# Kernel optimization log

Hardware: AMD Instinct MI355X
Metric: run time of the kernel (lower is better)

Reference implementation:

```python
import jax, jax.numpy as jnp
import numpy as np

N = 50000      # nodes
E = 800000     # edges (before self-loops)
IN_DIM = 128
HID = 96
PROJ = 64
BN_EPS = 1e-5
L2_EPS = 1e-12


def setup_inputs() -> dict:
    key = jax.random.key(0)
    ks = jax.random.split(key, 8)

    def glorot(k, shape):
        fan_in, fan_out = shape
        s = np.sqrt(6.0 / (fan_in + fan_out)).astype(np.float32)
        return jax.random.uniform(k, shape, jnp.float32, -s, s)

    x = jax.random.normal(ks[0], (N, IN_DIM), jnp.float32)
    edge_index = jax.random.randint(ks[1], (2, E), 0, N, dtype=jnp.int64)

    return {
        "x": x,
        "edge_index": edge_index,
        # GCN layer 1
        "W1": glorot(ks[2], (IN_DIM, HID)), "b1": jnp.zeros(HID, jnp.float32),
        "g1": jnp.ones(HID, jnp.float32), "be1": jnp.zeros(HID, jnp.float32),
        # GCN layer 2
        "W2": glorot(ks[3], (HID, HID)), "b2": jnp.zeros(HID, jnp.float32),
        "g2": jnp.ones(HID, jnp.float32), "be2": jnp.zeros(HID, jnp.float32),
        # projector: Linear -> BN -> ReLU -> Linear
        "Wp1": glorot(ks[4], (HID, HID)), "bp1": jnp.zeros(HID, jnp.float32),
        "gp": jnp.ones(HID, jnp.float32), "bep": jnp.zeros(HID, jnp.float32),
        "Wp2": glorot(ks[5], (HID, PROJ)), "bp2": jnp.zeros(PROJ, jnp.float32),
    }


def _batchnorm(h, gamma, beta):
    # training-mode BatchNorm1d: batch stats, biased variance
    m = h.mean(axis=0)
    v = h.var(axis=0)
    return gamma * (h - m) * jax.lax.rsqrt(v + BN_EPS) + beta


def _gcn_conv(x, W, b, src, dst, deg_inv_sqrt):
    # PyG GCNConv: x @ W, symmetric-normalized scatter-add (self-loops included
    # in src/dst), then bias.
    xw = x @ W                                              # [N, out]
    norm = deg_inv_sqrt[src] * deg_inv_sqrt[dst]            # [E+N]
    msg = xw[src] * norm[:, None]                           # [E+N, out]
    out = jax.ops.segment_sum(msg, dst, num_segments=x.shape[0])
    return out + b


def reference(x, edge_index, W1, b1, g1, be1, W2, b2, g2, be2,
              Wp1, bp1, gp, bep, Wp2, bp2):
    n = x.shape[0]
    loops = jnp.arange(n, dtype=edge_index.dtype)
    src = jnp.concatenate([edge_index[0], loops])
    dst = jnp.concatenate([edge_index[1], loops])
    deg = jax.ops.segment_sum(jnp.ones(src.shape[0], x.dtype), dst,
                              num_segments=n)               # includes self-loops
    deg_inv_sqrt = jax.lax.rsqrt(deg)                       # deg >= 1 always

    h = jax.nn.relu(_batchnorm(_gcn_conv(x, W1, b1, src, dst, deg_inv_sqrt), g1, be1))
    h = jax.nn.relu(_batchnorm(_gcn_conv(h, W2, b2, src, dst, deg_inv_sqrt), g2, be2))

    z = jax.nn.relu(_batchnorm(h @ Wp1 + bp1, gp, bep))
    z = z @ Wp2 + bp2
    # F.normalize(p=2, dim=-1, eps=1e-12)
    nrm = jnp.linalg.norm(z, axis=-1, keepdims=True)
    return z / jnp.maximum(nrm, L2_EPS)
```

## Files before the change

### kernel.cpp

```cpp
#include <hip/hip_runtime.h>
#include <hip/hip_fp16.h>

constexpr int BLK = 256;

static inline int cdiv(long long a, int b) { return (int)((a + b - 1) / b); }

using v8h = __attribute__((ext_vector_type(8))) _Float16;
using v4f = __attribute__((ext_vector_type(4))) float;


__global__ void zero_int(int* __restrict__ p, int n) {
    for (int i = blockIdx.x * blockDim.x + threadIdx.x; i < n; i += gridDim.x * blockDim.x)
        p[i] = 0;
}


__global__ void count_dst_off(const int* __restrict__ dst, int* __restrict__ cnt,
                              unsigned short* __restrict__ eoff, int E) {
    for (int i = blockIdx.x * blockDim.x + threadIdx.x; i < E; i += gridDim.x * blockDim.x)
        eoff[i] = (unsigned short)atomicAdd(&cnt[dst[i]], 1);
}

__global__ void scan1_dis(const int* __restrict__ cnt, int* __restrict__ rowptr,
                          int* __restrict__ bsum, float* __restrict__ dis, int N) {
    __shared__ int ts[256];
    int tid = threadIdx.x;
    int base = blockIdx.x * 1024 + tid * 4;
    int v[4], s = 0;
#pragma unroll
    for (int i = 0; i < 4; ++i) {
        v[i] = (base + i < N) ? cnt[base + i] : 0;
        s += v[i];
        if (base + i < N) dis[base + i] = rsqrtf((float)v[i] + 1.0f);
    }
    ts[tid] = s;
    __syncthreads();
    for (int off = 1; off < 256; off <<= 1) {
        int t = 0;
        if (tid >= off) t = ts[tid - off];
        __syncthreads();
        if (tid >= off) ts[tid] += t;
        __syncthreads();
    }
    int run = ts[tid] - s;
#pragma unroll
    for (int i = 0; i < 4; ++i) {
        if (base + i < N) rowptr[base + i] = run;
        run += v[i];
    }
    if (tid == 255) bsum[blockIdx.x] = ts[255];
}

__global__ void scan2z(const int* __restrict__ bsum, int* __restrict__ boff, int nb,
                       float* __restrict__ sums) {
    int tid = threadIdx.x;
    if (tid < 64) {
        int orig = (tid < nb) ? bsum[tid] : 0;
        int v = orig;
#pragma unroll
        for (int off = 1; off < 64; off <<= 1) {
            int t = __shfl_up(v, off, 64);
            if (tid >= off) v += t;
        }
        if (tid < nb) boff[tid] = v - orig;
    } else if (tid < 64 + 576) {
        sums[tid - 64] = 0.0f;
    }
}

__global__ void scan3(int* __restrict__ rowptr, const int* __restrict__ boff, int N, int E) {
    int i = blockIdx.x * blockDim.x + threadIdx.x;
    if (i < N) rowptr[i] += boff[i >> 10];
    if (i == 0) rowptr[N] = E;
}

__global__ void csr_fill(const int* __restrict__ src, const int* __restrict__ dst,
                         const unsigned short* __restrict__ eoff,
                         const int* __restrict__ rowptr,
                         unsigned short* __restrict__ csrc, int E) {
    for (int i = blockIdx.x * blockDim.x + threadIdx.x; i < E; i += gridDim.x * blockDim.x) {
        csrc[rowptr[dst[i]] + (int)eoff[i]] = (unsigned short)src[i];
    }
}


template <int K, bool ACT, bool BIAS, bool HOUT, bool WOUT, bool STATS>
__global__ __launch_bounds__(256) void gemm96m(const float* __restrict__ in,
                                               const float* __restrict__ W,
                                               const float* __restrict__ bias,
                                               const float* __restrict__ bnsums,
                                               const float* __restrict__ gamma,
                                               const float* __restrict__ beta,
                                               const float* __restrict__ dsc,
                                               float* __restrict__ out,
                                               _Float16* __restrict__ hout,
                                               float* __restrict__ osums, int N) {
    constexpr int NK = K / 32;
    constexpr int LDK = K + 8;
    __shared__ __align__(16) _Float16 Wt[96 * LDK];
    __shared__ __align__(16) float ssl[ACT ? 192 : 1];
    __shared__ float sb[STATS ? 192 : 1];
    const int tid = threadIdx.x;
    for (int idx = tid; idx < K * 96; idx += 256) {
        int k = idx / 96, n = idx - k * 96;
        Wt[n * LDK + k] = (_Float16)W[idx];
    }
    if (ACT && tid < 96) {
        float inv_n = 1.0f / (float)N;
        float mean = bnsums[tid] * inv_n;
        float var = bnsums[96 + tid] * inv_n - mean * mean;
        float sc = gamma[tid] * rsqrtf(var + 1e-5f);
        ssl[tid] = sc;
        ssl[96 + tid] = beta[tid] - mean * sc;
    }
    if (STATS && tid < 192) sb[tid] = 0.0f;
    __syncthreads();

    const int wave = tid >> 6, lane = tid & 63;
    const int quad = lane >> 4, lm = lane & 15;
    const int rbase = blockIdx.x * 64 + wave * 16;
    int arow = rbase + lm;
    arow = arow < N ? arow : N - 1;

    v8h afr[NK];
#pragma unroll
    for (int kc = 0; kc < NK; ++kc) {
        const float* p = &in[(long long)arow * K + kc * 32 + quad * 8];
        float4 p0 = *(const float4*)p;
        float4 p1 = *(const float4*)(p + 4);
        if (ACT) {
            int kk = kc * 32 + quad * 8;
            float4 sc0 = *(const float4*)&ssl[kk];
            float4 sc1 = *(const float4*)&ssl[kk + 4];
            float4 sh0 = *(const float4*)&ssl[96 + kk];
            float4 sh1 = *(const float4*)&ssl[96 + kk + 4];
            p0.x = fmaxf(fmaf(p0.x, sc0.x, sh0.x), 0.0f);
            p0.y = fmaxf(fmaf(p0.y, sc0.y, sh0.y), 0.0f);
            p0.z = fmaxf(fmaf(p0.z, sc0.z, sh0.z), 0.0f);
            p0.w = fmaxf(fmaf(p0.w, sc0.w, sh0.w), 0.0f);
            p1.x = fmaxf(fmaf(p1.x, sc1.x, sh1.x), 0.0f);
            p1.y = fmaxf(fmaf(p1.y, sc1.y, sh1.y), 0.0f);
            p1.z = fmaxf(fmaf(p1.z, sc1.z, sh1.z), 0.0f);
            p1.w = fmaxf(fmaf(p1.w, sc1.w, sh1.w), 0.0f);
        }
        v8h a;
        a[0] = (_Float16)p0.x; a[1] = (_Float16)p0.y;
        a[2] = (_Float16)p0.z; a[3] = (_Float16)p0.w;
        a[4] = (_Float16)p1.x; a[5] = (_Float16)p1.y;
        a[6] = (_Float16)p1.z; a[7] = (_Float16)p1.w;
        afr[kc] = a;
    }

    v4f acc[6];
#pragma unroll
    for (int t = 0; t < 6; ++t) {
        v4f c = {0.0f, 0.0f, 0.0f, 0.0f};
#pragma unroll
        for (int kc = 0; kc < NK; ++kc) {
            v8h b = *(const v8h*)&Wt[(t * 16 + lm) * LDK + kc * 32 + quad * 8];
            c = __builtin_amdgcn_mfma_f32_16x16x32_f16(afr[kc], b, c, 0, 0, 0);
        }
        acc[t] = c;
    }

    float dr[4];
    if (HOUT) {
#pragma unroll
        for (int r = 0; r < 4; ++r) {
            int gr = rbase + quad * 4 + r;
            dr[r] = dsc[gr < N ? gr : N - 1];
        }
    }

    float ls[6], lq[6];
#pragma unroll
    for (int t = 0; t < 6; ++t) { ls[t] = 0.0f; lq[t] = 0.0f; }
#pragma unroll
    for (int t = 0; t < 6; ++t) {
        float bv = BIAS ? bias[t * 16 + lm] : 0.0f;
#pragma unroll
        for (int r = 0; r < 4; ++r) {
            int gr = rbase + quad * 4 + r;
            if (gr < N) {
                float o = acc[t][r] + bv;
                if (WOUT) out[(long long)gr * 96 + t * 16 + lm] = o;
                if (HOUT) hout[(long long)gr * 96 + t * 16 + lm] = (_Float16)(o * dr[r]);
                if (STATS) { ls[t] += o; lq[t] += o * o; }
            }
        }
    }
    if (STATS) {
#pragma unroll
        for (int t = 0; t < 6; ++t) {
            ls[t] += __shfl_xor(ls[t], 16);
            ls[t] += __shfl_xor(ls[t], 32);
            lq[t] += __shfl_xor(lq[t], 16);
            lq[t] += __shfl_xor(lq[t], 32);
        }
        if (quad == 0) {
#pragma unroll
            for (int t = 0; t < 6; ++t) {
                atomicAdd(&sb[t * 16 + lm], ls[t]);
                atomicAdd(&sb[96 + t * 16 + lm], lq[t]);
            }
        }
        __syncthreads();
        if (tid < 192) atomicAdd(&osums[tid], sb[tid]);
    }
}


__global__ __launch_bounds__(256) void gemm_finalm(const float* __restrict__ in,
                                                   const float* __restrict__ W,
                                                   const float* __restrict__ bias,
                                                   const float* __restrict__ bnsums,
                                                   const float* __restrict__ gamma,
                                                   const float* __restrict__ beta,
                                                   float* __restrict__ out, int N) {
    constexpr int K = 96, NK = 3, LDK = K + 8;
    __shared__ __align__(16) _Float16 Wt[64 * LDK];
    __shared__ __align__(16) float ssl[192];
    const int tid = threadIdx.x;
    for (int idx = tid; idx < K * 64; idx += 256) {
        int k = idx / 64, n = idx - k * 64;
        Wt[n * LDK + k] = (_Float16)W[idx];
    }
    if (tid < 96) {
        float inv_n = 1.0f / (float)N;
        float mean = bnsums[tid] * inv_n;
        float var = bnsums[96 + tid] * inv_n - mean * mean;
        float sc = gamma[tid] * rsqrtf(var + 1e-5f);
        ssl[tid] = sc;
        ssl[96 + tid] = beta[tid] - mean * sc;
    }
    __syncthreads();

    const int wave = tid >> 6, lane = tid & 63;
    const int quad = lane >> 4, lm = lane & 15;
    const int rbase = blockIdx.x * 64 + wave * 16;
    int arow = rbase + lm;
    arow = arow < N ? arow : N - 1;

    v8h afr[NK];
#pragma unroll
    for (int kc = 0; kc < NK; ++kc) {
        const float* p = &in[(long long)arow * K + kc * 32 + quad * 8];
        float4 p0 = *(const float4*)p;
        float4 p1 = *(const float4*)(p + 4);
        int kk = kc * 32 + quad * 8;
        float4 sc0 = *(const float4*)&ssl[kk];
        float4 sc1 = *(const float4*)&ssl[kk + 4];
        float4 sh0 = *(const float4*)&ssl[96 + kk];
        float4 sh1 = *(const float4*)&ssl[96 + kk + 4];
        p0.x = fmaxf(fmaf(p0.x, sc0.x, sh0.x), 0.0f);
        p0.y = fmaxf(fmaf(p0.y, sc0.y, sh0.y), 0.0f);
        p0.z = fmaxf(fmaf(p0.z, sc0.z, sh0.z), 0.0f);
        p0.w = fmaxf(fmaf(p0.w, sc0.w, sh0.w), 0.0f);
        p1.x = fmaxf(fmaf(p1.x, sc1.x, sh1.x), 0.0f);
        p1.y = fmaxf(fmaf(p1.y, sc1.y, sh1.y), 0.0f);
        p1.z = fmaxf(fmaf(p1.z, sc1.z, sh1.z), 0.0f);
        p1.w = fmaxf(fmaf(p1.w, sc1.w, sh1.w), 0.0f);
        v8h a;
        a[0] = (_Float16)p0.x; a[1] = (_Float16)p0.y;
        a[2] = (_Float16)p0.z; a[3] = (_Float16)p0.w;
        a[4] = (_Float16)p1.x; a[5] = (_Float16)p1.y;
        a[6] = (_Float16)p1.z; a[7] = (_Float16)p1.w;
        afr[kc] = a;
    }

    v4f acc[4];
#pragma unroll
    for (int t = 0; t < 4; ++t) {
        v4f c = {0.0f, 0.0f, 0.0f, 0.0f};
#pragma unroll
        for (int kc = 0; kc < NK; ++kc) {
            v8h b = *(const v8h*)&Wt[(t * 16 + lm) * LDK + kc * 32 + quad * 8];
            c = __builtin_amdgcn_mfma_f32_16x16x32_f16(afr[kc], b, c, 0, 0, 0);
        }
        float bv = bias[t * 16 + lm];
        c[0] += bv; c[1] += bv; c[2] += bv; c[3] += bv;
        acc[t] = c;
    }

    float sq[4];
#pragma unroll
    for (int r = 0; r < 4; ++r) {
        float s = acc[0][r] * acc[0][r] + acc[1][r] * acc[1][r] +
                  acc[2][r] * acc[2][r] + acc[3][r] * acc[3][r];
#pragma unroll
        for (int m = 1; m < 16; m <<= 1) s += __shfl_xor(s, m, 64);
        sq[r] = 1.0f / fmaxf(sqrtf(s), 1e-12f);
    }
#pragma unroll
    for (int r = 0; r < 4; ++r) {
        int gr = rbase + quad * 4 + r;
        if (gr < N) {
#pragma unroll
            for (int t = 0; t < 4; ++t)
                out[(long long)gr * 64 + t * 16 + lm] = acc[t][r] * sq[r];
        }
    }
}


__device__ __forceinline__ void acc_row(float* acc, const __half2* h) {
#pragma unroll
    for (int k = 0; k < 4; ++k) {
        float2 f = __half22float2(h[k]);
        acc[2 * k + 0] += f.x;
        acc[2 * k + 1] += f.y;
    }
}

__global__ __launch_bounds__(256) void agg96h(const __half* __restrict__ hxw,
                                              const int* __restrict__ rowptr,
                                              const unsigned short* __restrict__ csrc,
                                              const float* __restrict__ dis,
                                              const float* __restrict__ bias,
                                              float* __restrict__ out, int N) {
    int idx = blockIdx.x * 256 + threadIdx.x;
    if (idx >= N * 12) return;
    int n = idx / 12, c8 = idx % 12;
    int ch = c8 * 8;
    float acc[8];
    {
        float4 g = *(const float4*)&hxw[(long long)n * 96 + ch];
        const __half2* hs = (const __half2*)&g;
#pragma unroll
        for (int k = 0; k < 4; ++k) {
            float2 f = __half22float2(hs[k]);
            acc[2 * k + 0] = f.x;
            acc[2 * k + 1] = f.y;
        }
    }
    int e = rowptr[n], e1 = rowptr[n + 1];
    for (; e + 7 < e1; e += 8) {
        int s[8];
        float4 g[8];
#pragma unroll
        for (int j = 0; j < 8; ++j) s[j] = csrc[e + j];
#pragma unroll
        for (int j = 0; j < 8; ++j)
            g[j] = *(const float4*)&hxw[(long long)s[j] * 96 + ch];
#pragma unroll
        for (int j = 0; j < 8; ++j) acc_row(acc, (const __half2*)&g[j]);
    }
    for (; e + 3 < e1; e += 4) {
        int s[4];
        float4 g[4];
#pragma unroll
        for (int j = 0; j < 4; ++j) s[j] = csrc[e + j];
#pragma unroll
        for (int j = 0; j < 4; ++j)
            g[j] = *(const float4*)&hxw[(long long)s[j] * 96 + ch];
#pragma unroll
        for (int j = 0; j < 4; ++j) acc_row(acc, (const __half2*)&g[j]);
    }
    for (; e < e1; ++e) {
        int s0 = csrc[e];
        float4 g0 = *(const float4*)&hxw[(long long)s0 * 96 + ch];
        acc_row(acc, (const __half2*)&g0);
    }
    float dn = dis[n];
    float4 o0, o1;
    o0.x = fmaf(acc[0], dn, bias[ch + 0]);
    o0.y = fmaf(acc[1], dn, bias[ch + 1]);
    o0.z = fmaf(acc[2], dn, bias[ch + 2]);
    o0.w = fmaf(acc[3], dn, bias[ch + 3]);
    o1.x = fmaf(acc[4], dn, bias[ch + 4]);
    o1.y = fmaf(acc[5], dn, bias[ch + 5]);
    o1.z = fmaf(acc[6], dn, bias[ch + 6]);
    o1.w = fmaf(acc[7], dn, bias[ch + 7]);
    *(float4*)&out[(long long)n * 96 + ch] = o0;
    *(float4*)&out[(long long)n * 96 + ch + 4] = o1;
}


__global__ __launch_bounds__(256) void bn_stats96(const float* __restrict__ h,
                                                  float* __restrict__ sums, int N) {
    __shared__ float sb[192];
    const int tid = threadIdx.x;
    if (tid < 192) sb[tid] = 0.0f;
    __syncthreads();
    int g = blockIdx.x * 256 + tid;
    int total = N * 24, stride = gridDim.x * 256;
    float4 s4 = {0, 0, 0, 0}, q4 = {0, 0, 0, 0};
    int c4 = g % 24;
    for (int i = g; i < total; i += stride) {
        int n = i / 24;
        float4 v = *(const float4*)&h[n * 96 + 4 * c4];
        s4.x += v.x; s4.y += v.y; s4.z += v.z; s4.w += v.w;
        q4.x += v.x * v.x; q4.y += v.y * v.y; q4.z += v.z * v.z; q4.w += v.w * v.w;
    }
    atomicAdd(&sb[4 * c4 + 0], s4.x);
    atomicAdd(&sb[4 * c4 + 1], s4.y);
    atomicAdd(&sb[4 * c4 + 2], s4.z);
    atomicAdd(&sb[4 * c4 + 3], s4.w);
    atomicAdd(&sb[96 + 4 * c4 + 0], q4.x);
    atomicAdd(&sb[96 + 4 * c4 + 1], q4.y);
    atomicAdd(&sb[96 + 4 * c4 + 2], q4.z);
    atomicAdd(&sb[96 + 4 * c4 + 3], q4.w);
    __syncthreads();
    if (tid < 192) atomicAdd(&sums[tid], sb[tid]);
}


extern "C" void kernel_launch(void* const* d_in, const int* in_sizes, int n_in,
                              void* d_out, int out_size, void* d_ws, size_t ws_size,
                              hipStream_t stream) {
    const float* x   = (const float*)d_in[0];
    const int*   ei  = (const int*)d_in[1];
    const float* W1  = (const float*)d_in[2];
    const float* b1  = (const float*)d_in[3];
    const float* g1  = (const float*)d_in[4];
    const float* be1 = (const float*)d_in[5];
    const float* W2  = (const float*)d_in[6];
    const float* b2  = (const float*)d_in[7];
    const float* g2  = (const float*)d_in[8];
    const float* be2 = (const float*)d_in[9];
    const float* Wp1 = (const float*)d_in[10];
    const float* bp1 = (const float*)d_in[11];
    const float* gp  = (const float*)d_in[12];
    const float* bep = (const float*)d_in[13];
    const float* Wp2 = (const float*)d_in[14];
    const float* bp2 = (const float*)d_in[15];

    const int N = in_sizes[0] / 128;
    const int E = in_sizes[1] / 2;
    const int* src = ei;
    const int* dst = ei + E;

    char* w = (char*)d_ws;
    auto alloc = [&](size_t bytes) { char* p = w; w += (bytes + 15) & ~size_t(15); return p; };
    int*            cnt    = (int*)alloc((size_t)N * 4);
    int*            rowptr = (int*)alloc((size_t)(N + 1) * 4);
    int*            bsum   = (int*)alloc(64 * 4);
    int*            boff   = (int*)alloc(64 * 4);
    float*          dis    = (float*)alloc((size_t)N * 4);
    unsigned short* eoff   = (unsigned short*)alloc((size_t)E * 2);
    unsigned short* csrc   = (unsigned short*)alloc((size_t)E * 2);
    float*          buf1   = (float*)alloc((size_t)N * 96 * 4);
    float*          buf2   = (float*)alloc((size_t)N * 96 * 4);
    _Float16*       hbuf   = (_Float16*)alloc((size_t)N * 96 * 2);
    float*          sums   = (float*)alloc(576 * 4);
    float* sums1 = sums, *sums2 = sums + 192, *sums3 = sums + 384;

    float* out = (float*)d_out;

    const int gE  = cdiv(E, BLK);
    const int gG  = cdiv(N, 64);
    const int gA  = cdiv((long long)N * 12, BLK);
    const int nb  = cdiv(N, 1024);

    zero_int<<<cdiv(N, BLK), BLK, 0, stream>>>(cnt, N);
    count_dst_off<<<gE, BLK, 0, stream>>>(dst, cnt, eoff, E);
    scan1_dis<<<nb, 256, 0, stream>>>(cnt, rowptr, bsum, dis, N);
    scan2z<<<1, 640, 0, stream>>>(bsum, boff, nb, sums);
    scan3<<<cdiv(N, BLK), BLK, 0, stream>>>(rowptr, boff, N, E);
    csr_fill<<<gE, BLK, 0, stream>>>(src, dst, eoff, rowptr, csrc, E);

    gemm96m<128, false, false, true, false, false><<<gG, 256, 0, stream>>>(
        x, W1, nullptr, nullptr, nullptr, nullptr, dis, nullptr, hbuf, nullptr, N);
    agg96h<<<gA, 256, 0, stream>>>((const __half*)hbuf, rowptr, csrc, dis, b1, buf2, N);
    bn_stats96<<<512, 256, 0, stream>>>(buf2, sums1, N);

    gemm96m<96, true, false, true, false, false><<<gG, 256, 0, stream>>>(
        buf2, W2, nullptr, sums1, g1, be1, dis, nullptr, hbuf, nullptr, N);
    agg96h<<<gA, 256, 0, stream>>>((const __half*)hbuf, rowptr, csrc, dis, b2, buf2, N);
    bn_stats96<<<512, 256, 0, stream>>>(buf2, sums2, N);

    gemm96m<96, true, true, false, true, true><<<gG, 256, 0, stream>>>(
        buf2, Wp1, bp1, sums2, g2, be2, nullptr, buf1, nullptr, sums3, N);

    gemm_finalm<<<gG, 256, 0, stream>>>(buf1, Wp2, bp2, sums3, gp, bep, out, N);
}
```

Before: 337.7 us.

## Fuse CSR build kernels into one cooperative kernel with grid syncs

Merges the six CSR-construction launches (zeroing, degree counting, three-phase scan, fill) into a single cooperative kernel of 512 blocks that separates the phases with grid-wide syncs. This is meant to cut per-kernel launch overhead and the gaps between small launches. The cost is five grid barriers and a fixed grid of 512 blocks striding over the work. The bn_stats grid size also changes from 512 to 510 blocks.

```diff
diff --git a/kernel.cpp b/kernel.cpp
--- a/kernel.cpp
+++ b/kernel.cpp
@@ -1,5 +1,8 @@
 #include <hip/hip_runtime.h>
 #include <hip/hip_fp16.h>
+#include <hip/hip_cooperative_groups.h>
+
+namespace cg = cooperative_groups;
 
 constexpr int BLK = 256;
 
@@ -9,52 +12,62 @@
 using v4f = __attribute__((ext_vector_type(4))) float;
 
 
-__global__ void zero_int(int* __restrict__ p, int n) {
-    for (int i = blockIdx.x * blockDim.x + threadIdx.x; i < n; i += gridDim.x * blockDim.x)
-        p[i] = 0;
-}
-
-
-__global__ void count_dst_off(const int* __restrict__ dst, int* __restrict__ cnt,
-                              unsigned short* __restrict__ eoff, int E) {
-    for (int i = blockIdx.x * blockDim.x + threadIdx.x; i < E; i += gridDim.x * blockDim.x)
+__global__ __launch_bounds__(256) void csr_build(const int* __restrict__ src,
+                                                 const int* __restrict__ dst,
+                                                 int* __restrict__ cnt,
+                                                 int* __restrict__ rowptr,
+                                                 int* __restrict__ bsum,
+                                                 int* __restrict__ boff,
+                                                 float* __restrict__ dis,
+                                                 unsigned short* __restrict__ eoff,
+                                                 unsigned short* __restrict__ csrc,
+                                                 float* __restrict__ sums,
+                                                 int N, int E) {
+    cg::grid_group grid = cg::this_grid();
+    const int tid = threadIdx.x;
+    const int gid = blockIdx.x * blockDim.x + tid;
+    const int gsz = gridDim.x * blockDim.x;
+    const int nb = (N + 1023) >> 10;
+    __shared__ int ts[256];
+
+    for (int i = gid; i < N; i += gsz) cnt[i] = 0;
+    if (gid < 576) sums[gid] = 0.0f;
+    grid.sync();
+
+    for (int i = gid; i < E; i += gsz)
         eoff[i] = (unsigned short)atomicAdd(&cnt[dst[i]], 1);
-}
-
-__global__ void scan1_dis(const int* __restrict__ cnt, int* __restrict__ rowptr,
-                          int* __restrict__ bsum, float* __restrict__ dis, int N) {
-    __shared__ int ts[256];
-    int tid = threadIdx.x;
-    int base = blockIdx.x * 1024 + tid * 4;
-    int v[4], s = 0;
-#pragma unroll
-    for (int i = 0; i < 4; ++i) {
-        v[i] = (base + i < N) ? cnt[base + i] : 0;
-        s += v[i];
-        if (base + i < N) dis[base + i] = rsqrtf((float)v[i] + 1.0f);
-    }
-    ts[tid] = s;
-    __syncthreads();
-    for (int off = 1; off < 256; off <<= 1) {
-        int t = 0;
-        if (tid >= off) t = ts[tid - off];
+    grid.sync();
+
+    for (int b = blockIdx.x; b < nb; b += gridDim.x) {
+        int base = b * 1024 + tid * 4;
+        int v[4], s = 0;
+#pragma unroll
+        for (int i = 0; i < 4; ++i) {
+            v[i] = (base + i < N) ? cnt[base + i] : 0;
+            s += v[i];
+            if (base + i < N) dis[base + i] = rsqrtf((float)v[i] + 1.0f);
+        }
+        ts[tid] = s;
         __syncthreads();
-        if (tid >= off) ts[tid] += t;
+        for (int off = 1; off < 256; off <<= 1) {
+            int t = 0;
+            if (tid >= off) t = ts[tid - off];
+            __syncthreads();
+            if (tid >= off) ts[tid] += t;
+            __syncthreads();
+        }
+        int run = ts[tid] - s;
+#pragma unroll
+        for (int i = 0; i < 4; ++i) {
+            if (base + i < N) rowptr[base + i] = run;
+            run += v[i];
+        }
+        if (tid == 255) bsum[b] = ts[255];
         __syncthreads();
     }
-    int run = ts[tid] - s;
-#pragma unroll
-    for (int i = 0; i < 4; ++i) {
-        if (base + i < N) rowptr[base + i] = run;
-        run += v[i];
-    }
-    if (tid == 255) bsum[blockIdx.x] = ts[255];
-}
-
-__global__ void scan2z(const int* __restrict__ bsum, int* __restrict__ boff, int nb,
-                       float* __restrict__ sums) {
-    int tid = threadIdx.x;
-    if (tid < 64) {
+    grid.sync();
+
+    if (blockIdx.x == 0 && tid < 64) {
         int orig = (tid < nb) ? bsum[tid] : 0;
         int v = orig;
 #pragma unroll
@@ -63,24 +76,15 @@
             if (tid >= off) v += t;
         }
         if (tid < nb) boff[tid] = v - orig;
-    } else if (tid < 64 + 576) {
-        sums[tid - 64] = 0.0f;
-    }
-}
-
-__global__ void scan3(int* __restrict__ rowptr, const int* __restrict__ boff, int N, int E) {
-    int i = blockIdx.x * blockDim.x + threadIdx.x;
-    if (i < N) rowptr[i] += boff[i >> 10];
-    if (i == 0) rowptr[N] = E;
-}
-
-__global__ void csr_fill(const int* __restrict__ src, const int* __restrict__ dst,
-                         const unsigned short* __restrict__ eoff,
-                         const int* __restrict__ rowptr,
-                         unsigned short* __restrict__ csrc, int E) {
-    for (int i = blockIdx.x * blockDim.x + threadIdx.x; i < E; i += gridDim.x * blockDim.x) {
+    }
+    grid.sync();
+
+    for (int i = gid; i < N; i += gsz) rowptr[i] += boff[i >> 10];
+    if (gid == 0) rowptr[N] = E;
+    grid.sync();
+
+    for (int i = gid; i < E; i += gsz)
         csrc[rowptr[dst[i]] + (int)eoff[i]] = (unsigned short)src[i];
-    }
 }
 
 
@@ -447,27 +451,27 @@
 
     float* out = (float*)d_out;
 
-    const int gE  = cdiv(E, BLK);
     const int gG  = cdiv(N, 64);
     const int gA  = cdiv((long long)N * 12, BLK);
-    const int nb  = cdiv(N, 1024);
-
-    zero_int<<<cdiv(N, BLK), BLK, 0, stream>>>(cnt, N);
-    count_dst_off<<<gE, BLK, 0, stream>>>(dst, cnt, eoff, E);
-    scan1_dis<<<nb, 256, 0, stream>>>(cnt, rowptr, bsum, dis, N);
-    scan2z<<<1, 640, 0, stream>>>(bsum, boff, nb, sums);
-    scan3<<<cdiv(N, BLK), BLK, 0, stream>>>(rowptr, boff, N, E);
-    csr_fill<<<gE, BLK, 0, stream>>>(src, dst, eoff, rowptr, csrc, E);
+
+    {
+        int Nv = N, Ev = E;
+        void* args[] = {(void*)&src, (void*)&dst, (void*)&cnt, (void*)&rowptr,
+                        (void*)&bsum, (void*)&boff, (void*)&dis, (void*)&eoff,
+                        (void*)&csrc, (void*)&sums, (void*)&Nv, (void*)&Ev};
+        hipLaunchCooperativeKernel((const void*)csr_build, dim3(512), dim3(256),
+                                   args, 0, stream);
+    }
 
     gemm96m<128, false, false, true, false, false><<<gG, 256, 0, stream>>>(
         x, W1, nullptr, nullptr, nullptr, nullptr, dis, nullptr, hbuf, nullptr, N);
     agg96h<<<gA, 256, 0, stream>>>((const __half*)hbuf, rowptr, csrc, dis, b1, buf2, N);
-    bn_stats96<<<512, 256, 0, stream>>>(buf2, sums1, N);
+    bn_stats96<<<510, 256, 0, stream>>>(buf2, sums1, N);
 
     gemm96m<96, true, false, true, false, false><<<gG, 256, 0, stream>>>(
         buf2, W2, nullptr, sums1, g1, be1, dis, nullptr, hbuf, nullptr, N);
     agg96h<<<gA, 256, 0, stream>>>((const __half*)hbuf, rowptr, csrc, dis, b2, buf2, N);
-    bn_stats96<<<512, 256, 0, stream>>>(buf2, sums2, N);
+    bn_stats96<<<510, 256, 0, stream>>>(buf2, sums2, N);
 
     gemm96m<96, true, true, false, true, true><<<gG, 256, 0, stream>>>(
         buf2, Wp1, bp1, sums2, g2, be2, nullptr, buf1, nullptr, sums3, N);
```

New measurement: 618.6 us. 1.83x slower.

## Fuse layer-1 GEMM with zeroing and apply degree scaling inside aggregation

Applied to the files above, without the earlier changes.

The first GEMM no longer depends on the degree vector. It runs at the start, fused with zeroing the counters and BN sums, so it is independent of the CSR build. The layer-1 aggregation instead reads dis[src] per edge and applies that weight on the fly. The two scan passes merge into one kernel that recomputes the block offsets in shared memory, cutting launch count. The cost is an extra gather of dis per edge in the first aggregation, and the block-offset prefix is repeated in every scan block.

```diff
diff --git a/kernel.cpp b/kernel.cpp
--- a/kernel.cpp
+++ b/kernel.cpp
@@ -7,12 +7,6 @@
 
 using v8h = __attribute__((ext_vector_type(8))) _Float16;
 using v4f = __attribute__((ext_vector_type(4))) float;
-
-
-__global__ void zero_int(int* __restrict__ p, int n) {
-    for (int i = blockIdx.x * blockDim.x + threadIdx.x; i < n; i += gridDim.x * blockDim.x)
-        p[i] = 0;
-}
 
 
 __global__ void count_dst_off(const int* __restrict__ dst, int* __restrict__ cnt,
@@ -21,8 +15,10 @@
         eoff[i] = (unsigned short)atomicAdd(&cnt[dst[i]], 1);
 }
 
-__global__ void scan1_dis(const int* __restrict__ cnt, int* __restrict__ rowptr,
-                          int* __restrict__ bsum, float* __restrict__ dis, int N) {
+__global__ __launch_bounds__(256) void scan1_dis(const int* __restrict__ cnt,
+                                                 int* __restrict__ rowptr,
+                                                 int* __restrict__ bsum,
+                                                 float* __restrict__ dis, int N) {
     __shared__ int ts[256];
     int tid = threadIdx.x;
     int base = blockIdx.x * 1024 + tid * 4;
@@ -51,9 +47,11 @@
     if (tid == 255) bsum[blockIdx.x] = ts[255];
 }
 
-__global__ void scan2z(const int* __restrict__ bsum, int* __restrict__ boff, int nb,
-                       float* __restrict__ sums) {
-    int tid = threadIdx.x;
+__global__ __launch_bounds__(256) void scan23(int* __restrict__ rowptr,
+                                              const int* __restrict__ bsum,
+                                              int nb, int N, int E) {
+    __shared__ int sboff[64];
+    const int tid = threadIdx.x;
     if (tid < 64) {
         int orig = (tid < nb) ? bsum[tid] : 0;
         int v = orig;
@@ -62,15 +60,11 @@
             int t = __shfl_up(v, off, 64);
             if (tid >= off) v += t;
         }
-        if (tid < nb) boff[tid] = v - orig;
-    } else if (tid < 64 + 576) {
-        sums[tid - 64] = 0.0f;
-    }
-}
-
-__global__ void scan3(int* __restrict__ rowptr, const int* __restrict__ boff, int N, int E) {
-    int i = blockIdx.x * blockDim.x + threadIdx.x;
-    if (i < N) rowptr[i] += boff[i >> 10];
+        sboff[tid] = v - orig;
+    }
+    __syncthreads();
+    int i = blockIdx.x * 256 + tid;
+    if (i < N) rowptr[i] += sboff[i >> 10];
     if (i == 0) rowptr[N] = E;
 }
 
@@ -85,16 +79,17 @@
 
 
 template <int K, bool ACT, bool BIAS, bool HOUT, bool WOUT, bool STATS>
-__global__ __launch_bounds__(256) void gemm96m(const float* __restrict__ in,
-                                               const float* __restrict__ W,
-                                               const float* __restrict__ bias,
-                                               const float* __restrict__ bnsums,
-                                               const float* __restrict__ gamma,
-                                               const float* __restrict__ beta,
-                                               const float* __restrict__ dsc,
-                                               float* __restrict__ out,
-                                               _Float16* __restrict__ hout,
-                                               float* __restrict__ osums, int N) {
+__device__ __forceinline__ void gemm96_body(int bid,
+                                            const float* __restrict__ in,
+                                            const float* __restrict__ W,
+                                            const float* __restrict__ bias,
+                                            const float* __restrict__ bnsums,
+                                            const float* __restrict__ gamma,
+                                            const float* __restrict__ beta,
+                                            const float* __restrict__ dsc,
+                                            float* __restrict__ out,
+                                            _Float16* __restrict__ hout,
+                                            float* __restrict__ osums, int N) {
     constexpr int NK = K / 32;
     constexpr int LDK = K + 8;
     __shared__ __align__(16) _Float16 Wt[96 * LDK];
@@ -118,7 +113,7 @@
 
     const int wave = tid >> 6, lane = tid & 63;
     const int quad = lane >> 4, lm = lane & 15;
-    const int rbase = blockIdx.x * 64 + wave * 16;
+    const int rbase = bid * 64 + wave * 16;
     int arow = rbase + lm;
     arow = arow < N ? arow : N - 1;
 
@@ -168,7 +163,7 @@
 #pragma unroll
         for (int r = 0; r < 4; ++r) {
             int gr = rbase + quad * 4 + r;
-            dr[r] = dsc[gr < N ? gr : N - 1];
+            dr[r] = dsc ? dsc[gr < N ? gr : N - 1] : 1.0f;
         }
     }
 
@@ -206,6 +201,39 @@
         }
         __syncthreads();
         if (tid < 192) atomicAdd(&osums[tid], sb[tid]);
+    }
+}
+
+template <int K, bool ACT, bool BIAS, bool HOUT, bool WOUT, bool STATS>
+__global__ __launch_bounds__(256) void gemm96m(const float* __restrict__ in,
+                                               const float* __restrict__ W,
+                                               const float* __restrict__ bias,
+                                               const float* __restrict__ bnsums,
+                                               const float* __restrict__ gamma,
+                                               const float* __restrict__ beta,
+                                               const float* __restrict__ dsc,
+                                               float* __restrict__ out,
+                                               _Float16* __restrict__ hout,
+                                               float* __restrict__ osums, int N) {
+    gemm96_body<K, ACT, BIAS, HOUT, WOUT, STATS>(blockIdx.x, in, W, bias, bnsums,
+                                                 gamma, beta, dsc, out, hout, osums, N);
+}
+
+__global__ __launch_bounds__(256) void gemm1_zero(const float* __restrict__ x,
+                                                  const float* __restrict__ W1,
+                                                  _Float16* __restrict__ hout,
+                                                  int* __restrict__ cnt,
+                                                  float* __restrict__ sums,
+                                                  int gG, int N) {
+    if ((int)blockIdx.x < gG) {
+        gemm96_body<128, false, false, true, false, false>(
+            blockIdx.x, x, W1, nullptr, nullptr, nullptr, nullptr, nullptr,
+            nullptr, hout, nullptr, N);
+    } else {
+        int g = (blockIdx.x - gG) * 256 + threadIdx.x;
+        int stride = (gridDim.x - gG) * 256;
+        for (int i = g; i < N; i += stride) cnt[i] = 0;
+        if (g < 576) sums[g] = 0.0f;
     }
 }
 
@@ -312,6 +340,16 @@
     }
 }
 
+__device__ __forceinline__ void acc_roww(float* acc, const __half2* h, float w) {
+#pragma unroll
+    for (int k = 0; k < 4; ++k) {
+        float2 f = __half22float2(h[k]);
+        acc[2 * k + 0] = fmaf(f.x, w, acc[2 * k + 0]);
+        acc[2 * k + 1] = fmaf(f.y, w, acc[2 * k + 1]);
+    }
+}
+
+template <bool PRESC>
 __global__ __launch_bounds__(256) void agg96h(const __half* __restrict__ hxw,
                                               const int* __restrict__ rowptr,
                                               const unsigned short* __restrict__ csrc,
@@ -322,46 +360,64 @@
     if (idx >= N * 12) return;
     int n = idx / 12, c8 = idx % 12;
     int ch = c8 * 8;
+    float dn = dis[n];
     float acc[8];
     {
+        float sw = PRESC ? 1.0f : dn;
         float4 g = *(const float4*)&hxw[(long long)n * 96 + ch];
         const __half2* hs = (const __half2*)&g;
 #pragma unroll
         for (int k = 0; k < 4; ++k) {
             float2 f = __half22float2(hs[k]);
-            acc[2 * k + 0] = f.x;
-            acc[2 * k + 1] = f.y;
+            acc[2 * k + 0] = f.x * sw;
+            acc[2 * k + 1] = f.y * sw;
         }
     }
     int e = rowptr[n], e1 = rowptr[n + 1];
     for (; e + 7 < e1; e += 8) {
         int s[8];
         float4 g[8];
+        float w[8];
 #pragma unroll
         for (int j = 0; j < 8; ++j) s[j] = csrc[e + j];
+        if (!PRESC) {
+#pragma unroll
+            for (int j = 0; j < 8; ++j) w[j] = dis[s[j]];
+        }
 #pragma unroll
         for (int j = 0; j < 8; ++j)
             g[j] = *(const float4*)&hxw[(long long)s[j] * 96 + ch];
 #pragma unroll
-        for (int j = 0; j < 8; ++j) acc_row(acc, (const __half2*)&g[j]);
+        for (int j = 0; j < 8; ++j) {
+            if (PRESC) acc_row(acc, (const __half2*)&g[j]);
+            else       acc_roww(acc, (const __half2*)&g[j], w[j]);
+        }
     }
     for (; e + 3 < e1; e += 4) {
         int s[4];
         float4 g[4];
+        float w[4];
 #pragma unroll
         for (int j = 0; j < 4; ++j) s[j] = csrc[e + j];
+        if (!PRESC) {
+#pragma unroll
+            for (int j = 0; j < 4; ++j) w[j] = dis[s[j]];
+        }
 #pragma unroll
         for (int j = 0; j < 4; ++j)
             g[j] = *(const float4*)&hxw[(long long)s[j] * 96 + ch];
 #pragma unroll
-        for (int j = 0; j < 4; ++j) acc_row(acc, (const __half2*)&g[j]);
+        for (int j = 0; j < 4; ++j) {
+            if (PRESC) acc_row(acc, (const __half2*)&g[j]);
+            else       acc_roww(acc, (const __half2*)&g[j], w[j]);
+        }
     }
     for (; e < e1; ++e) {
         int s0 = csrc[e];
         float4 g0 = *(const float4*)&hxw[(long long)s0 * 96 + ch];
-        acc_row(acc, (const __half2*)&g0);
-    }
-    float dn = dis[n];
+        if (PRESC) acc_row(acc, (const __half2*)&g0);
+        else       acc_roww(acc, (const __half2*)&g0, dis[s0]);
+    }
     float4 o0, o1;
     o0.x = fmaf(acc[0], dn, bias[ch + 0]);
     o0.y = fmaf(acc[1], dn, bias[ch + 1]);
@@ -435,7 +491,6 @@
     int*            cnt    = (int*)alloc((size_t)N * 4);
     int*            rowptr = (int*)alloc((size_t)(N + 1) * 4);
     int*            bsum   = (int*)alloc(64 * 4);
-    int*            boff   = (int*)alloc(64 * 4);
     float*          dis    = (float*)alloc((size_t)N * 4);
     unsigned short* eoff   = (unsigned short*)alloc((size_t)E * 2);
     unsigned short* csrc   = (unsigned short*)alloc((size_t)E * 2);
@@ -452,22 +507,21 @@
     const int gA  = cdiv((long long)N * 12, BLK);
     const int nb  = cdiv(N, 1024);
 
-    zero_int<<<cdiv(N, BLK), BLK, 0, stream>>>(cnt, N);
+    gemm1_zero<<<gG + nb, 256, 0, stream>>>(x, W1, hbuf, cnt, sums, gG, N);
     count_dst_off<<<gE, BLK, 0, stream>>>(dst, cnt, eoff, E);
     scan1_dis<<<nb, 256, 0, stream>>>(cnt, rowptr, bsum, dis, N);
-    scan2z<<<1, 640, 0, stream>>>(bsum, boff, nb, sums);
-    scan3<<<cdiv(N, BLK), BLK, 0, stream>>>(rowptr, boff, N, E);
+    scan23<<<cdiv(N, 256), 256, 0, stream>>>(rowptr, bsum, nb, N, E);
     csr_fill<<<gE, BLK, 0, stream>>>(src, dst, eoff, rowptr, csrc, E);
 
-    gemm96m<128, false, false, true, false, false><<<gG, 256, 0, stream>>>(
-        x, W1, nullptr, nullptr, nullptr, nullptr, dis, nullptr, hbuf, nullptr, N);
-    agg96h<<<gA, 256, 0, stream>>>((const __half*)hbuf, rowptr, csrc, dis, b1, buf2, N);
-    bn_stats96<<<512, 256, 0, stream>>>(buf2, sums1, N);
+    agg96h<false><<<gA, 256, 0, stream>>>((const __half*)hbuf, rowptr, csrc, dis,
+                                          b1, buf2, N);
+    bn_stats96<<<510, 256, 0, stream>>>(buf2, sums1, N);
 
     gemm96m<96, true, false, true, false, false><<<gG, 256, 0, stream>>>(
         buf2, W2, nullptr, sums1, g1, be1, dis, nullptr, hbuf, nullptr, N);
-    agg96h<<<gA, 256, 0, stream>>>((const __half*)hbuf, rowptr, csrc, dis, b2, buf2, N);
-    bn_stats96<<<512, 256, 0, stream>>>(buf2, sums2, N);
+    agg96h<true><<<gA, 256, 0, stream>>>((const __half*)hbuf, rowptr, csrc, dis,
+                                         b2, buf2, N);
+    bn_stats96<<<510, 256, 0, stream>>>(buf2, sums2, N);
 
     gemm96m<96, true, true, false, true, true><<<gG, 256, 0, stream>>>(
         buf2, Wp1, bp1, sums2, g2, be2, nullptr, buf1, nullptr, sums3, N);
```

Result: no change. 333.7 us (-1.2%).
